# Performance work log

Hardware: AMD Instinct MI355X
Metric: run time of the kernel (lower is better)

## Reference

```python
import jax, jax.numpy as jnp
import numpy as np

C = 256
D = C // 4  # shared q/k projection dim = 64
EPS_BN = 1e-5


def _bn(x, g, b, m, v):
    # inference-style BatchNorm1d over channel dim of [B, C, N]
    inv = g / jnp.sqrt(v + EPS_BN)
    return x * inv[:, None] + (b - m * inv)[:, None]


def _sa_layer(x, xyz, qk_w, v_w, v_b, tr_w, tr_b, g, b, m, var):
    h = x + xyz                                             # [B,C,N]
    q = jnp.einsum('dc,bcn->bnd', qk_w, h)                  # [B,N,D]
    k = jnp.einsum('dc,bcn->bdn', qk_w, h)                  # [B,D,N] (shared weight)
    v = jnp.einsum('oc,bcn->bon', v_w, h) + v_b[:, None]    # [B,C,N]
    energy = jnp.einsum('bnd,bdm->bnm', q, k)               # [B,N,N]
    att = jax.nn.softmax(energy, axis=-1)
    # offset-attention L1 renorm over query dim (dim=1)
    att = att / (1e-9 + att.sum(axis=1, keepdims=True))
    x_r = jnp.einsum('bcn,bnm->bcm', v, att)                # [B,C,N]
    t = jnp.einsum('oc,bcn->bon', tr_w, x - x_r) + tr_b[:, None]
    return x + jax.nn.relu(_bn(t, g, b, m, var))


def setup_inputs() -> dict:
    key = jax.random.key(0)
    ks = jax.random.split(key, 20)
    B, N = 4, 4096
    inp = {
        'x': jax.random.normal(ks[0], (B, C, N), jnp.float32),
        'xyz': jax.random.normal(ks[1], (B, N, 3), jnp.float32),
        'pos_w': jax.random.normal(ks[2], (C, 3), jnp.float32) * 0.1,
        'pos_b': jax.random.normal(ks[3], (C,), jnp.float32) * 0.05,
        'conv1_w': jax.random.normal(ks[4], (C, C), jnp.float32) * (1.0 / np.sqrt(C)),
        'bn1_g': jax.random.uniform(ks[5], (C,), jnp.float32, 0.5, 1.5),
        'bn1_b': jax.random.normal(ks[6], (C,), jnp.float32) * 0.05,
        'bn1_m': jax.random.normal(ks[7], (C,), jnp.float32) * 0.05,
        'bn1_v': jax.random.uniform(ks[8], (C,), jnp.float32, 0.5, 1.5),
        # stacked params for 4 SA layers
        'qk_w': jax.random.normal(ks[9], (4, D, C), jnp.float32) * (1.0 / np.sqrt(C)),
        'v_w': jax.random.normal(ks[10], (4, C, C), jnp.float32) * (1.0 / np.sqrt(C)),
        'v_b': jax.random.normal(ks[11], (4, C), jnp.float32) * 0.05,
        'tr_w': jax.random.normal(ks[12], (4, C, C), jnp.float32) * (1.0 / np.sqrt(C)),
        'tr_b': jax.random.normal(ks[13], (4, C), jnp.float32) * 0.05,
        'bn_g': jax.random.uniform(ks[14], (4, C), jnp.float32, 0.5, 1.5),
        'bn_b': jax.random.normal(ks[15], (4, C), jnp.float32) * 0.05,
        'bn_m': jax.random.normal(ks[16], (4, C), jnp.float32) * 0.05,
        'bn_v': jax.random.uniform(ks[17], (4, C), jnp.float32, 0.5, 1.5),
    }
    return inp


def reference(x, xyz, pos_w, pos_b, conv1_w, bn1_g, bn1_b, bn1_m, bn1_v,
              qk_w, v_w, v_b, tr_w, tr_b, bn_g, bn_b, bn_m, bn_v):
    # xyz: [B,N,3] -> permute -> [B,3,N] -> pos conv -> [B,C,N]
    pos = jnp.einsum('oc,bnc->bon', pos_w, xyz) + pos_b[:, None]
    h = jnp.einsum('oc,bcn->bon', conv1_w, x)
    h = jax.nn.relu(_bn(h, bn1_g, bn1_b, bn1_m, bn1_v))
    outs = []
    for i in range(4):
        h = _sa_layer(h, pos, qk_w[i], v_w[i], v_b[i], tr_w[i], tr_b[i],
                      bn_g[i], bn_b[i], bn_m[i], bn_v[i])
        outs.append(h)
    return jnp.concatenate(outs, axis=1)  # [B, 4C, N]
```

## Files before the change

### kernel.cpp

```cpp
#include <hip/hip_runtime.h>

#define NB 4
#define NC 256
#define ND 64
#define NN 4096

typedef unsigned short us;
using short8v = __attribute__((ext_vector_type(8))) short;
using f32x4   = __attribute__((ext_vector_type(4))) float;

#define MFMA16 __builtin_amdgcn_mfma_f32_16x16x32_bf16

constexpr size_t SBCN = (size_t)NB * NC * NN;
constexpr size_t SBN  = (size_t)NB * NN;

__device__ inline us f2bf(float f) {
  unsigned u = __builtin_bit_cast(unsigned, f);
  u += 0x7fffu + ((u >> 16) & 1u);
  return (us)(u >> 16);
}
__device__ inline float bf2f(us s) {
  unsigned u = (unsigned)s << 16;
  return __builtin_bit_cast(float, u);
}
__device__ inline unsigned pack2(float a, float b) {
  return (unsigned)f2bf(a) | ((unsigned)f2bf(b) << 16);
}

__global__ __launch_bounds__(256) void pos_kernel(
    const float* __restrict__ xyz, const float* __restrict__ pw,
    const float* __restrict__ pb, float* __restrict__ pos)
{
  int idx = blockIdx.x * 256 + threadIdx.x;
  int n  = idx & (NN - 1);
  int tc = idx >> 12;
  int o  = tc & (NC - 1);
  int b  = tc >> 8;
  const float* xp = xyz + ((size_t)b * NN + n) * 3;
  pos[idx] = pb[o] + pw[o*3+0]*xp[0] + pw[o*3+1]*xp[1] + pw[o*3+2]*xp[2];
}

template<int O, bool ADD_P, bool HAS_BIAS, bool HAS_BN, bool RELU,
         bool HAS_RES, bool TRIPLE, bool VSPLIT, bool HAS_OUT2>
__global__ __launch_bounds__(256) void wgemm(
    const float* __restrict__ W, const float* __restrict__ H,
    const float* __restrict__ P, const float* __restrict__ bias,
    const float* __restrict__ bng, const float* __restrict__ bnb,
    const float* __restrict__ bnm, const float* __restrict__ bnv,
    const float* __restrict__ RES, float* __restrict__ OUT,
    float* __restrict__ OUT2, float* __restrict__ OUT3,
    float* __restrict__ OUT4)
{
  __shared__ float Wt[16][64];
  __shared__ float Ht[16][64];
  const int b  = blockIdx.z;
  const int o0 = blockIdx.y * 64;
  const int n0 = blockIdx.x * 64;
  const int t  = threadIdx.x;
  const int og = t >> 4, ng = t & 15;
  const int lo = t >> 2, lc4 = (t & 3) * 4;
  const int hc = t >> 4, hn4 = (t & 15) * 4;
  float acc[4][4] = {};
  for (int c0 = 0; c0 < NC; c0 += 16) {
    float4 w4 = *(const float4*)&W[(size_t)(o0 + lo) * NC + c0 + lc4];
    float4 h4 = *(const float4*)&H[((size_t)b * NC + c0 + hc) * NN + n0 + hn4];
    if (ADD_P) {
      float4 p4 = *(const float4*)&P[((size_t)b * NC + c0 + hc) * NN + n0 + hn4];
      h4.x += p4.x; h4.y += p4.y; h4.z += p4.z; h4.w += p4.w;
    }
    Wt[lc4+0][lo] = w4.x; Wt[lc4+1][lo] = w4.y;
    Wt[lc4+2][lo] = w4.z; Wt[lc4+3][lo] = w4.w;
    *(float4*)&Ht[hc][hn4] = h4;
    __syncthreads();
    #pragma unroll
    for (int cc = 0; cc < 16; ++cc) {
      float4 wv = *(const float4*)&Wt[cc][og*4];
      float4 hv = *(const float4*)&Ht[cc][ng*4];
      float wa[4] = {wv.x, wv.y, wv.z, wv.w};
      float ha[4] = {hv.x, hv.y, hv.z, hv.w};
      #pragma unroll
      for (int i = 0; i < 4; ++i)
        #pragma unroll
        for (int j = 0; j < 4; ++j)
          acc[i][j] += wa[i] * ha[j];
    }
    __syncthreads();
  }
  float vals[4][4];
  #pragma unroll
  for (int i = 0; i < 4; ++i) {
    const int o = o0 + og * 4 + i;
    float sc = 1.0f, sh = 0.0f;
    if (HAS_BIAS) sh = bias[o];
    if (HAS_BN) {
      float inv = bng[o] * rsqrtf(bnv[o] + 1e-5f);
      sh = sh * inv + (bnb[o] - bnm[o] * inv);
      sc = inv;
    }
    #pragma unroll
    for (int j = 0; j < 4; ++j) {
      float v = acc[i][j] * sc + sh;
      if (RELU) v = fmaxf(v, 0.0f);
      vals[i][j] = v;
    }
    if (HAS_RES) {
      float4 rv = *(const float4*)&RES[((size_t)b * NC + o) * NN + n0 + ng*4];
      vals[i][0] += rv.x; vals[i][1] += rv.y;
      vals[i][2] += rv.z; vals[i][3] += rv.w;
    }
  }
  if (TRIPLE) {
    us* o1 = (us*)OUT;  us* o2 = (us*)OUT2;  us* o3 = (us*)OUT3;
    #pragma unroll
    for (int j = 0; j < 4; ++j) {
      const int n = n0 + ng * 4 + j;
      us s1[4], s2[4], s3[4];
      #pragma unroll
      for (int i = 0; i < 4; ++i) {
        float v = vals[i][j];
        us h1 = f2bf(v); float r = v - bf2f(h1);
        us h2 = f2bf(r); r -= bf2f(h2);
        us h3 = f2bf(r);
        s1[i] = h1; s2[i] = h2; s3[i] = h3;
      }
      const size_t base = ((size_t)b * NN + n) * 64 + og * 4;
      uint2 u;
      u.x = (unsigned)s1[0] | ((unsigned)s1[1] << 16);
      u.y = (unsigned)s1[2] | ((unsigned)s1[3] << 16);
      *(uint2*)&o1[base] = u;
      u.x = (unsigned)s2[0] | ((unsigned)s2[1] << 16);
      u.y = (unsigned)s2[2] | ((unsigned)s2[3] << 16);
      *(uint2*)&o2[base] = u;
      u.x = (unsigned)s3[0] | ((unsigned)s3[1] << 16);
      u.y = (unsigned)s3[2] | ((unsigned)s3[3] << 16);
      *(uint2*)&o3[base] = u;
    }
  } else if (VSPLIT) {
    us* v1p = (us*)OUT; us* v2p = (us*)OUT2;
    #pragma unroll
    for (int i = 0; i < 4; ++i) {
      const int o = o0 + og * 4 + i;
      us s1[4], s2[4];
      #pragma unroll
      for (int j = 0; j < 4; ++j) {
        float v = vals[i][j];
        us h1 = f2bf(v);
        s1[j] = h1;
        s2[j] = f2bf(v - bf2f(h1));
      }
      const size_t base = ((size_t)b * NC + o) * NN + n0 + ng * 4;
      uint2 u;
      u.x = (unsigned)s1[0] | ((unsigned)s1[1] << 16);
      u.y = (unsigned)s1[2] | ((unsigned)s1[3] << 16);
      *(uint2*)&v1p[base] = u;
      u.x = (unsigned)s2[0] | ((unsigned)s2[1] << 16);
      u.y = (unsigned)s2[2] | ((unsigned)s2[3] << 16);
      *(uint2*)&v2p[base] = u;
    }
  } else {
    #pragma unroll
    for (int i = 0; i < 4; ++i) {
      const int o = o0 + og * 4 + i;
      float4 r = {vals[i][0], vals[i][1], vals[i][2], vals[i][3]};
      *(float4*)&OUT[((size_t)b * O + o) * NN + n0 + ng*4] = r;
      if (HAS_OUT2)
        *(float4*)&OUT2[((size_t)b * 4 * NC + o) * NN + n0 + ng*4] = r;
    }
  }
}

__global__ __launch_bounds__(128, 3) void rowstats_mfma(
    const us* __restrict__ q1, const us* __restrict__ q2,
    const us* __restrict__ q3,
    float* __restrict__ Mr, float* __restrict__ Lr)
{
  __shared__ us qs[3][32][72];
  const int b = blockIdx.y;
  const int n0 = blockIdx.x * 32;
  const int t = threadIdx.x;
  const int w = t >> 6, l = t & 63, lm = l & 15, g = l >> 4;
  const int nrow = n0 + w * 16;
  const us* qp[3] = {q1, q2, q3};
  short8v an[3][2];
  #pragma unroll
  for (int s = 0; s < 3; ++s) {
    const size_t ab = ((size_t)b * NN + nrow + lm) * ND + 8 * g;
    an[s][0] = *(const short8v*)(qp[s] + ab);
    an[s][1] = *(const short8v*)(qp[s] + ab + 32);
  }
  float mrun[4], lrun[4];
  #pragma unroll
  for (int r = 0; r < 4; ++r) { mrun[r] = -1e30f; lrun[r] = 0.f; }

  const int nloc0 = t >> 3, d8 = (t & 7) * 8;
  for (int m0 = 0; m0 < NN; m0 += 32) {
    __syncthreads();
    #pragma unroll
    for (int i = 0; i < 6; ++i) {
      const int s = i >> 1, n = (i & 1) * 16 + nloc0;
      *(short8v*)&qs[s][n][d8] =
          *(const short8v*)(qp[s] + ((size_t)b * NN + m0 + n) * ND + d8);
    }
    __syncthreads();
    float e[2][4];
    #pragma unroll
    for (int sub = 0; sub < 2; ++sub) {
      f32x4 eA = {0.f,0.f,0.f,0.f}, eB = {0.f,0.f,0.f,0.f};
      #pragma unroll
      for (int kh = 0; kh < 2; ++kh) {
        short8v b0 = *(const short8v*)&qs[0][sub*16+lm][kh*32+8*g];
        short8v b1 = *(const short8v*)&qs[1][sub*16+lm][kh*32+8*g];
        short8v b2 = *(const short8v*)&qs[2][sub*16+lm][kh*32+8*g];
        eA = MFMA16(an[0][kh], b0, eA, 0,0,0);
        eA = MFMA16(an[0][kh], b1, eA, 0,0,0);
        eA = MFMA16(an[0][kh], b2, eA, 0,0,0);
        eB = MFMA16(an[1][kh], b0, eB, 0,0,0);
        eB = MFMA16(an[2][kh], b0, eB, 0,0,0);
        eB = MFMA16(an[1][kh], b1, eB, 0,0,0);
      }
      f32x4 ee = eA + eB;
      #pragma unroll
      for (int r = 0; r < 4; ++r) e[sub][r] = ee[r];
    }
    #pragma unroll
    for (int r = 0; r < 4; ++r) {
      float mx = fmaxf(e[0][r], e[1][r]);
      float p = __expf(e[0][r] - mx) + __expf(e[1][r] - mx);
      float d = mx - mrun[r];
      if (d > 8.f) { lrun[r] = lrun[r] * __expf(-d) + p; mrun[r] = mx; }
      else          lrun[r] += p * __expf(d);
    }
  }
  #pragma unroll
  for (int r = 0; r < 4; ++r) {
    float m = mrun[r], s = lrun[r];
    #pragma unroll
    for (int off = 1; off < 16; off <<= 1) {
      float om = __shfl_xor(m, off);
      float os = __shfl_xor(s, off);
      float nm = fmaxf(m, om);
      s = s * __expf(m - nm) + os * __expf(om - nm);
      m = nm;
    }
    if (lm == 0) {
      Mr[(size_t)b * NN + nrow + 4 * g + r] = m;
      Lr[(size_t)b * NN + nrow + 4 * g + r] = 1.0f / s;
    }
  }
}

__global__ __launch_bounds__(256, 4) void fusedatt_mfma(
    const us* __restrict__ q1, const us* __restrict__ q2,
    const us* __restrict__ q3,
    const us* __restrict__ v1, const us* __restrict__ v2,
    const float* __restrict__ Mr, const float* __restrict__ Lr,
    float* __restrict__ xr, float* __restrict__ csb)
{
  __shared__ us qs[2][3][32][72];
  __shared__ us att1[64][40];
  __shared__ us att2[64][40];
  const int b  = blockIdx.y;
  const int m0 = blockIdx.x * 64;
  const int chalf = blockIdx.z & 1;
  const int nk    = blockIdx.z >> 1;
  const int c0 = chalf * 128;
  const int t  = threadIdx.x;
  const int w  = t >> 6, l = t & 63, lm = l & 15, g = l >> 4;
  const int mrow = w * 16 + lm;
  const int mg   = m0 + mrow;
  const us* qp[3] = {q1, q2, q3};

  short8v bm[3][2];
  #pragma unroll
  for (int s = 0; s < 3; ++s) {
    const size_t mb = ((size_t)b * NN + mg) * ND + 8 * g;
    bm[s][0] = *(const short8v*)(qp[s] + mb);
    bm[s][1] = *(const short8v*)(qp[s] + mb + 32);
  }
  const float* Mb = Mr + (size_t)b * NN;
  const float* Lb = Lr + (size_t)b * NN;
  const us* vb1 = v1 + ((size_t)b * NC + c0 + w * 32 + lm) * NN + 8 * g;
  const us* vb2 = v2 + ((size_t)b * NC + c0 + w * 32 + lm) * NN + 8 * g;

  f32x4 acc[2][4];
  const f32x4 fzero = {0.f,0.f,0.f,0.f};
  #pragma unroll
  for (int cs = 0; cs < 2; ++cs)
    #pragma unroll
    for (int mm = 0; mm < 4; ++mm) acc[cs][mm] = fzero;
  float csp = 0.f;

  const int nloc = t >> 3, d8 = (t & 7) * 8;
  const int nbeg = nk * (NN / 2), nend = nbeg + NN / 2;

  #pragma unroll
  for (int i = 0; i < 3; ++i)
    *(short8v*)&qs[0][i][nloc][d8] =
        *(const short8v*)(qp[i] + ((size_t)b * NN + nbeg + nloc) * ND + d8);
  __syncthreads();

  int cur = 0;
  for (int nt = nbeg; nt < nend; nt += 32) {
    short8v nx0, nx1, nx2;
    const bool has_next = (nt + 32) < nend;
    if (has_next) {
      const size_t nb = ((size_t)b * NN + nt + 32 + nloc) * ND + d8;
      nx0 = *(const short8v*)(qp[0] + nb);
      nx1 = *(const short8v*)(qp[1] + nb);
      nx2 = *(const short8v*)(qp[2] + nb);
    }
    #pragma unroll
    for (int sub = 0; sub < 2; ++sub) {
      f32x4 eA = fzero, eB = fzero;
      #pragma unroll
      for (int kh = 0; kh < 2; ++kh) {
        short8v a0 = *(const short8v*)&qs[cur][0][sub*16+lm][kh*32+8*g];
        short8v a1 = *(const short8v*)&qs[cur][1][sub*16+lm][kh*32+8*g];
        short8v a2 = *(const short8v*)&qs[cur][2][sub*16+lm][kh*32+8*g];
        eA = MFMA16(a0, bm[0][kh], eA, 0,0,0);
        eA = MFMA16(a0, bm[1][kh], eA, 0,0,0);
        eA = MFMA16(a0, bm[2][kh], eA, 0,0,0);
        eB = MFMA16(a1, bm[0][kh], eB, 0,0,0);
        eB = MFMA16(a2, bm[0][kh], eB, 0,0,0);
        eB = MFMA16(a1, bm[1][kh], eB, 0,0,0);
      }
      f32x4 ee = eA + eB;
      float m4[4], l4[4];
      *(float4*)m4 = *(const float4*)&Mb[nt + sub*16 + 4*g];
      *(float4*)l4 = *(const float4*)&Lb[nt + sub*16 + 4*g];
      us a1r[4], a2r[4];
      #pragma unroll
      for (int r = 0; r < 4; ++r) {
        float p = __expf(ee[r] - m4[r]) * l4[r];
        csp += p;
        us hi = f2bf(p);
        a1r[r] = hi;
        a2r[r] = f2bf(p - bf2f(hi));
      }
      uint2 u;
      u.x = (unsigned)a1r[0] | ((unsigned)a1r[1] << 16);
      u.y = (unsigned)a1r[2] | ((unsigned)a1r[3] << 16);
      *(uint2*)&att1[mrow][sub*16 + 4*g] = u;
      u.x = (unsigned)a2r[0] | ((unsigned)a2r[1] << 16);
      u.y = (unsigned)a2r[2] | ((unsigned)a2r[3] << 16);
      *(uint2*)&att2[mrow][sub*16 + 4*g] = u;
    }
    if (has_next) {
      *(short8v*)&qs[cur ^ 1][0][nloc][d8] = nx0;
      *(short8v*)&qs[cur ^ 1][1][nloc][d8] = nx1;
      *(short8v*)&qs[cur ^ 1][2][nloc][d8] = nx2;
    }
    __syncthreads();
    #pragma unroll
    for (int cs = 0; cs < 2; ++cs) {
      short8v av1 = *(const short8v*)(vb1 + (size_t)cs * 16 * NN + nt);
      short8v av2 = *(const short8v*)(vb2 + (size_t)cs * 16 * NN + nt);
      #pragma unroll
      for (int mm = 0; mm < 4; ++mm) {
        short8v batt1 = *(const short8v*)&att1[mm * 16 + lm][8 * g];
        short8v batt2 = *(const short8v*)&att2[mm * 16 + lm][8 * g];
        acc[cs][mm] = MFMA16(av1, batt1, acc[cs][mm], 0,0,0);
        acc[cs][mm] = MFMA16(av2, batt1, acc[cs][mm], 0,0,0);
        acc[cs][mm] = MFMA16(av1, batt2, acc[cs][mm], 0,0,0);
      }
    }
    __syncthreads();
    cur ^= 1;
  }

  csp += __shfl_xor(csp, 16);
  csp += __shfl_xor(csp, 32);
  if (chalf == 0 && l < 16)
    csb[(size_t)nk * SBN + (size_t)b * NN + m0 + w * 16 + l] = csp;

  float* xrp = xr + (size_t)nk * SBCN;
  #pragma unroll
  for (int cs = 0; cs < 2; ++cs) {
    #pragma unroll
    for (int mm = 0; mm < 4; ++mm) {
      #pragma unroll
      for (int r = 0; r < 4; ++r) {
        const int c = c0 + w * 32 + cs * 16 + 4 * g + r;
        const int m = m0 + mm * 16 + lm;
        xrp[((size_t)b * NC + c) * NN + m] = acc[cs][mm][r];
      }
    }
  }
}

__global__ __launch_bounds__(256) void xr_reduce(
    const float* __restrict__ xr, const float* __restrict__ csb,
    const float* __restrict__ h, float* __restrict__ dbuf)
{
  const int i4 = blockIdx.x * 256 + threadIdx.x;
  const int mq = i4 & (NN / 4 - 1);
  const int bc = i4 >> 10;
  const int b  = bc >> 8;
  const size_t off = (size_t)bc * NN + mq * 4;
  float4 a0 = *(const float4*)&xr[off];
  float4 a1 = *(const float4*)&xr[SBCN + off];
  float4 hv = *(const float4*)&h[off];
  const size_t co = (size_t)b * NN + mq * 4;
  float4 c0 = *(const float4*)&csb[co];
  float4 c1 = *(const float4*)&csb[SBN + co];
  float4 r;
  r.x = hv.x - (a0.x + a1.x) / (1e-9f + c0.x + c1.x);
  r.y = hv.y - (a0.y + a1.y) / (1e-9f + c0.y + c1.y);
  r.z = hv.z - (a0.z + a1.z) / (1e-9f + c0.z + c1.z);
  r.w = hv.w - (a0.w + a1.w) / (1e-9f + c0.w + c1.w);
  *(float4*)&dbuf[off] = r;
}

extern "C" void kernel_launch(void* const* d_in, const int* in_sizes, int n_in,
                              void* d_out, int out_size, void* d_ws, size_t ws_size,
                              hipStream_t stream) {
  const float* x      = (const float*)d_in[0];
  const float* xyz    = (const float*)d_in[1];
  const float* pos_w  = (const float*)d_in[2];
  const float* pos_b  = (const float*)d_in[3];
  const float* conv1w = (const float*)d_in[4];
  const float* bn1_g  = (const float*)d_in[5];
  const float* bn1_b  = (const float*)d_in[6];
  const float* bn1_m  = (const float*)d_in[7];
  const float* bn1_v  = (const float*)d_in[8];
  const float* qk_w   = (const float*)d_in[9];
  const float* v_w    = (const float*)d_in[10];
  const float* v_b    = (const float*)d_in[11];
  const float* tr_w   = (const float*)d_in[12];
  const float* tr_b   = (const float*)d_in[13];
  const float* bn_g   = (const float*)d_in[14];
  const float* bn_b   = (const float*)d_in[15];
  const float* bn_m   = (const float*)d_in[16];
  const float* bn_v   = (const float*)d_in[17];
  float* out = (float*)d_out;
  float* ws  = (float*)d_ws;

  const size_t BCN = SBCN;
  const size_t BDN = (size_t)NB * ND * NN;
  const size_t BN  = SBN;
  float* pos  = ws;
  float* h    = pos + BCN;
  float* xr   = h   + BCN;
  float* Mr   = xr  + 2 * BCN;
  float* Lr   = Mr  + BN;
  float* csb  = Lr  + BN;
  us* qA1 = (us*)(csb + 2 * BN);
  us* qA2 = qA1 + BDN;
  us* qA3 = qA2 + BDN;
  us* v1  = qA3 + BDN;
  us* v2  = v1  + BCN;

  pos_kernel<<<(NB * NC * NN) / 256, 256, 0, stream>>>(xyz, pos_w, pos_b, pos);

  wgemm<256, false, false, true, true, false, false, false, false>
      <<<dim3(NN/64, NC/64, NB), 256, 0, stream>>>(
          conv1w, x, nullptr, nullptr, bn1_g, bn1_b, bn1_m, bn1_v,
          nullptr, h, nullptr, nullptr, nullptr);

  for (int li = 0; li < 4; ++li) {
    const float* qw = qk_w + (size_t)li * ND * NC;
    const float* vw = v_w  + (size_t)li * NC * NC;
    const float* vb = v_b  + (size_t)li * NC;
    const float* tw = tr_w + (size_t)li * NC * NC;
    const float* tb = tr_b + (size_t)li * NC;

    wgemm<64, true, false, false, false, false, true, false, false>
        <<<dim3(NN/64, 1, NB), 256, 0, stream>>>(
            qw, h, pos, nullptr, nullptr, nullptr, nullptr, nullptr,
            nullptr, (float*)qA1, (float*)qA2, (float*)qA3, nullptr);

    wgemm<256, true, true, false, false, false, false, true, false>
        <<<dim3(NN/64, NC/64, NB), 256, 0, stream>>>(
            vw, h, pos, vb, nullptr, nullptr, nullptr, nullptr,
            nullptr, (float*)v1, (float*)v2, nullptr, nullptr);

    rowstats_mfma<<<dim3(NN/32, NB), 128, 0, stream>>>(qA1, qA2, qA3, Mr, Lr);

    fusedatt_mfma<<<dim3(NN/64, NB, 4), 256, 0, stream>>>(
        qA1, qA2, qA3, v1, v2, Mr, Lr, xr, csb);

    xr_reduce<<<(unsigned)(BCN / 1024), 256, 0, stream>>>(xr, csb, h, xr);

    wgemm<256, false, true, true, true, true, false, false, true>
        <<<dim3(NN/64, NC/64, NB), 256, 0, stream>>>(
            tw, xr, nullptr, tb, bn_g + li*NC, bn_b + li*NC,
            bn_m + li*NC, bn_v + li*NC,
            h, h, out + (size_t)li * NC * NN, nullptr, nullptr);
  }
}
```

Baseline: 1.850 ms.

## Move q/v/trans projections to bf16x3 split MFMA GEMMs with fused splits

Replaces the fp32 SIMT tiled GEMMs for the q, v and trans projections with an MFMA kernel. It uses three-way bf16 splits of both weights and activations, with six cross-product MFMAs per tile to keep near-fp32 accuracy. Weights are split once up front. Activations are transposed and split into n-major bf16 buffers by a new tsplit kernel, and that kernel absorbs the old xr_reduce normalization. The trans GEMM epilogue writes h and the output slice, and also emits the split (h+pos) operand for the next layer, aliasing the xr workspace. The cost is extra split-buffer memory traffic and a few extra launches, in exchange for running the projection math on matrix cores instead of vector FMAs.

```diff
diff --git a/kernel.cpp b/kernel.cpp
--- a/kernel.cpp
+++ b/kernel.cpp
@@ -22,9 +22,6 @@
 __device__ inline float bf2f(us s) {
   unsigned u = (unsigned)s << 16;
   return __builtin_bit_cast(float, u);
-}
-__device__ inline unsigned pack2(float a, float b) {
-  return (unsigned)f2bf(a) | ((unsigned)f2bf(b) << 16);
 }
 
 __global__ __launch_bounds__(256) void pos_kernel(
@@ -40,16 +37,11 @@
   pos[idx] = pb[o] + pw[o*3+0]*xp[0] + pw[o*3+1]*xp[1] + pw[o*3+2]*xp[2];
 }
 
-template<int O, bool ADD_P, bool HAS_BIAS, bool HAS_BN, bool RELU,
-         bool HAS_RES, bool TRIPLE, bool VSPLIT, bool HAS_OUT2>
-__global__ __launch_bounds__(256) void wgemm(
+__global__ __launch_bounds__(256) void wgemm_conv1(
     const float* __restrict__ W, const float* __restrict__ H,
-    const float* __restrict__ P, const float* __restrict__ bias,
     const float* __restrict__ bng, const float* __restrict__ bnb,
     const float* __restrict__ bnm, const float* __restrict__ bnv,
-    const float* __restrict__ RES, float* __restrict__ OUT,
-    float* __restrict__ OUT2, float* __restrict__ OUT3,
-    float* __restrict__ OUT4)
+    float* __restrict__ OUT)
 {
   __shared__ float Wt[16][64];
   __shared__ float Ht[16][64];
@@ -64,10 +56,6 @@
   for (int c0 = 0; c0 < NC; c0 += 16) {
     float4 w4 = *(const float4*)&W[(size_t)(o0 + lo) * NC + c0 + lc4];
     float4 h4 = *(const float4*)&H[((size_t)b * NC + c0 + hc) * NN + n0 + hn4];
-    if (ADD_P) {
-      float4 p4 = *(const float4*)&P[((size_t)b * NC + c0 + hc) * NN + n0 + hn4];
-      h4.x += p4.x; h4.y += p4.y; h4.z += p4.z; h4.w += p4.w;
-    }
     Wt[lc4+0][lo] = w4.x; Wt[lc4+1][lo] = w4.y;
     Wt[lc4+2][lo] = w4.z; Wt[lc4+3][lo] = w4.w;
     *(float4*)&Ht[hc][hn4] = h4;
@@ -86,44 +74,158 @@
     }
     __syncthreads();
   }
-  float vals[4][4];
   #pragma unroll
   for (int i = 0; i < 4; ++i) {
     const int o = o0 + og * 4 + i;
-    float sc = 1.0f, sh = 0.0f;
-    if (HAS_BIAS) sh = bias[o];
-    if (HAS_BN) {
-      float inv = bng[o] * rsqrtf(bnv[o] + 1e-5f);
-      sh = sh * inv + (bnb[o] - bnm[o] * inv);
-      sc = inv;
-    }
-    #pragma unroll
-    for (int j = 0; j < 4; ++j) {
-      float v = acc[i][j] * sc + sh;
-      if (RELU) v = fmaxf(v, 0.0f);
-      vals[i][j] = v;
-    }
-    if (HAS_RES) {
-      float4 rv = *(const float4*)&RES[((size_t)b * NC + o) * NN + n0 + ng*4];
-      vals[i][0] += rv.x; vals[i][1] += rv.y;
-      vals[i][2] += rv.z; vals[i][3] += rv.w;
-    }
-  }
-  if (TRIPLE) {
-    us* o1 = (us*)OUT;  us* o2 = (us*)OUT2;  us* o3 = (us*)OUT3;
-    #pragma unroll
-    for (int j = 0; j < 4; ++j) {
-      const int n = n0 + ng * 4 + j;
+    float inv = bng[o] * rsqrtf(bnv[o] + 1e-5f);
+    float sh = bnb[o] - bnm[o] * inv;
+    float4 r;
+    r.x = fmaxf(acc[i][0]*inv + sh, 0.f);
+    r.y = fmaxf(acc[i][1]*inv + sh, 0.f);
+    r.z = fmaxf(acc[i][2]*inv + sh, 0.f);
+    r.w = fmaxf(acc[i][3]*inv + sh, 0.f);
+    *(float4*)&OUT[((size_t)b * NC + o) * NN + n0 + ng*4] = r;
+  }
+}
+
+__global__ __launch_bounds__(256) void wsplit(
+    const float* __restrict__ src, us* __restrict__ d1,
+    us* __restrict__ d2, us* __restrict__ d3, int ntot)
+{
+  int i = blockIdx.x * 256 + threadIdx.x;
+  if (i >= ntot) return;
+  float v = src[i];
+  us h1 = f2bf(v); float r = v - bf2f(h1);
+  us h2 = f2bf(r); r -= bf2f(h2);
+  us h3 = f2bf(r);
+  d1[i] = h1; d2[i] = h2; d3[i] = h3;
+}
+
+template<bool FROM_XR>
+__global__ __launch_bounds__(256) void tsplit(
+    const float* __restrict__ h, const float* __restrict__ pos,
+    const float* __restrict__ xr, const float* __restrict__ csb,
+    us* __restrict__ o1, us* __restrict__ o2, us* __restrict__ o3)
+{
+  __shared__ float tile[64][69];
+  __shared__ float cf[64];
+  const int b = blockIdx.z, c0 = blockIdx.y * 64, n0 = blockIdx.x * 64;
+  const int t = threadIdx.x;
+  if (FROM_XR) {
+    if (t < 64) {
+      const size_t co = (size_t)b * NN + n0 + t;
+      cf[t] = 1.0f / (1e-9f + csb[co] + csb[SBN + co]);
+    }
+    __syncthreads();
+  }
+  #pragma unroll
+  for (int p = 0; p < 4; ++p) {
+    const int c = p * 16 + (t >> 4), n4 = (t & 15) * 4;
+    const size_t off = ((size_t)b * NC + c0 + c) * NN + n0 + n4;
+    float4 hv = *(const float4*)&h[off];
+    float v0, v1, v2, v3;
+    if (FROM_XR) {
+      float4 a0 = *(const float4*)&xr[off];
+      float4 a1 = *(const float4*)&xr[SBCN + off];
+      v0 = hv.x - (a0.x + a1.x) * cf[n4+0];
+      v1 = hv.y - (a0.y + a1.y) * cf[n4+1];
+      v2 = hv.z - (a0.z + a1.z) * cf[n4+2];
+      v3 = hv.w - (a0.w + a1.w) * cf[n4+3];
+    } else {
+      float4 pv = *(const float4*)&pos[off];
+      v0 = hv.x + pv.x; v1 = hv.y + pv.y;
+      v2 = hv.z + pv.z; v3 = hv.w + pv.w;
+    }
+    tile[c][n4+0] = v0; tile[c][n4+1] = v1;
+    tile[c][n4+2] = v2; tile[c][n4+3] = v3;
+  }
+  __syncthreads();
+  const int w = t >> 6, l = t & 63;
+  const int n = w * 16 + (l >> 2), cq = (l & 3) * 16;
+  #pragma unroll
+  for (int j = 0; j < 4; ++j) {
+    const int c4 = cq + j * 4;
+    us s1[4], s2[4], s3[4];
+    #pragma unroll
+    for (int i = 0; i < 4; ++i) {
+      float v = tile[c4 + i][n];
+      us h1 = f2bf(v); float r = v - bf2f(h1);
+      us h2 = f2bf(r); r -= bf2f(h2);
+      s1[i] = h1; s2[i] = h2; s3[i] = f2bf(r);
+    }
+    const size_t base = ((size_t)b * NN + n0 + n) * NC + c0 + c4;
+    uint2 u;
+    u.x = (unsigned)s1[0] | ((unsigned)s1[1] << 16);
+    u.y = (unsigned)s1[2] | ((unsigned)s1[3] << 16);
+    *(uint2*)&o1[base] = u;
+    u.x = (unsigned)s2[0] | ((unsigned)s2[1] << 16);
+    u.y = (unsigned)s2[2] | ((unsigned)s2[3] << 16);
+    *(uint2*)&o2[base] = u;
+    u.x = (unsigned)s3[0] | ((unsigned)s3[1] << 16);
+    u.y = (unsigned)s3[2] | ((unsigned)s3[3] << 16);
+    *(uint2*)&o3[base] = u;
+  }
+}
+
+template<bool QOUT, bool VOUT, bool TROUT>
+__global__ __launch_bounds__(256, 4) void mgemm(
+    const us* __restrict__ w1, const us* __restrict__ w2,
+    const us* __restrict__ w3,
+    const us* __restrict__ i1, const us* __restrict__ i2,
+    const us* __restrict__ i3,
+    const float* __restrict__ bias,
+    const float* __restrict__ bng, const float* __restrict__ bnb,
+    const float* __restrict__ bnm, const float* __restrict__ bnv,
+    const float* __restrict__ RES, const float* __restrict__ pos,
+    float* __restrict__ hout, float* __restrict__ outsl,
+    us* __restrict__ o1, us* __restrict__ o2, us* __restrict__ o3)
+{
+  const int b  = blockIdx.z;
+  const int o0 = blockIdx.y * 64;
+  const int n0 = blockIdx.x * 64;
+  const int t  = threadIdx.x;
+  const int w  = t >> 6, l = t & 63, lm = l & 15, g = l >> 4;
+  const int n  = n0 + w * 16 + lm;
+  const size_t ibase = ((size_t)b * NN + n) * 256 + 8 * g;
+
+  f32x4 acc[4];
+  const f32x4 fzero = {0.f,0.f,0.f,0.f};
+  #pragma unroll
+  for (int osub = 0; osub < 4; ++osub) acc[osub] = fzero;
+
+  #pragma unroll
+  for (int kh = 0; kh < 8; ++kh) {
+    const int ko = kh * 32;
+    short8v bh1 = *(const short8v*)(i1 + ibase + ko);
+    short8v bh2 = *(const short8v*)(i2 + ibase + ko);
+    short8v bh3 = *(const short8v*)(i3 + ibase + ko);
+    #pragma unroll
+    for (int osub = 0; osub < 4; ++osub) {
+      const size_t wb = (size_t)(o0 + osub * 16 + lm) * 256 + ko + 8 * g;
+      short8v aw1 = *(const short8v*)(w1 + wb);
+      short8v aw2 = *(const short8v*)(w2 + wb);
+      short8v aw3 = *(const short8v*)(w3 + wb);
+      acc[osub] = MFMA16(aw1, bh1, acc[osub], 0,0,0);
+      acc[osub] = MFMA16(aw1, bh2, acc[osub], 0,0,0);
+      acc[osub] = MFMA16(aw2, bh1, acc[osub], 0,0,0);
+      acc[osub] = MFMA16(aw1, bh3, acc[osub], 0,0,0);
+      acc[osub] = MFMA16(aw2, bh2, acc[osub], 0,0,0);
+      acc[osub] = MFMA16(aw3, bh1, acc[osub], 0,0,0);
+    }
+  }
+
+  #pragma unroll
+  for (int osub = 0; osub < 4; ++osub) {
+    if (QOUT) {
       us s1[4], s2[4], s3[4];
       #pragma unroll
-      for (int i = 0; i < 4; ++i) {
-        float v = vals[i][j];
-        us h1 = f2bf(v); float r = v - bf2f(h1);
-        us h2 = f2bf(r); r -= bf2f(h2);
-        us h3 = f2bf(r);
-        s1[i] = h1; s2[i] = h2; s3[i] = h3;
-      }
-      const size_t base = ((size_t)b * NN + n) * 64 + og * 4;
+      for (int r = 0; r < 4; ++r) {
+        float v = acc[osub][r];
+        us h1 = f2bf(v); float rr = v - bf2f(h1);
+        us h2 = f2bf(rr); rr -= bf2f(h2);
+        s1[r] = h1; s2[r] = h2; s3[r] = f2bf(rr);
+      }
+      const size_t base = ((size_t)b * NN + n) * 64 + osub * 16 + 4 * g;
       uint2 u;
       u.x = (unsigned)s1[0] | ((unsigned)s1[1] << 16);
       u.y = (unsigned)s1[2] | ((unsigned)s1[3] << 16);
@@ -134,37 +236,43 @@
       u.x = (unsigned)s3[0] | ((unsigned)s3[1] << 16);
       u.y = (unsigned)s3[2] | ((unsigned)s3[3] << 16);
       *(uint2*)&o3[base] = u;
-    }
-  } else if (VSPLIT) {
-    us* v1p = (us*)OUT; us* v2p = (us*)OUT2;
-    #pragma unroll
-    for (int i = 0; i < 4; ++i) {
-      const int o = o0 + og * 4 + i;
-      us s1[4], s2[4];
-      #pragma unroll
-      for (int j = 0; j < 4; ++j) {
-        float v = vals[i][j];
+    } else if (VOUT) {
+      #pragma unroll
+      for (int r = 0; r < 4; ++r) {
+        const int c = o0 + osub * 16 + 4 * g + r;
+        float v = acc[osub][r] + bias[c];
         us h1 = f2bf(v);
-        s1[j] = h1;
-        s2[j] = f2bf(v - bf2f(h1));
-      }
-      const size_t base = ((size_t)b * NC + o) * NN + n0 + ng * 4;
+        const size_t off = ((size_t)b * NC + c) * NN + n;
+        o1[off] = h1;
+        o2[off] = f2bf(v - bf2f(h1));
+      }
+    } else {
+      us s1[4], s2[4], s3[4];
+      #pragma unroll
+      for (int r = 0; r < 4; ++r) {
+        const int c = o0 + osub * 16 + 4 * g + r;
+        const size_t off = ((size_t)b * NC + c) * NN + n;
+        float inv = bng[c] * rsqrtf(bnv[c] + 1e-5f);
+        float sh = bias[c] * inv + (bnb[c] - bnm[c] * inv);
+        float val = fmaxf(acc[osub][r] * inv + sh, 0.f) + RES[off];
+        hout[off] = val;
+        outsl[((size_t)b * 4 * NC + c) * NN + n] = val;
+        float hpv = val + pos[off];
+        us h1 = f2bf(hpv); float rr = hpv - bf2f(h1);
+        us h2 = f2bf(rr); rr -= bf2f(h2);
+        s1[r] = h1; s2[r] = h2; s3[r] = f2bf(rr);
+      }
+      const size_t base = ((size_t)b * NN + n) * NC + o0 + osub * 16 + 4 * g;
       uint2 u;
       u.x = (unsigned)s1[0] | ((unsigned)s1[1] << 16);
       u.y = (unsigned)s1[2] | ((unsigned)s1[3] << 16);
-      *(uint2*)&v1p[base] = u;
+      *(uint2*)&o1[base] = u;
       u.x = (unsigned)s2[0] | ((unsigned)s2[1] << 16);
       u.y = (unsigned)s2[2] | ((unsigned)s2[3] << 16);
-      *(uint2*)&v2p[base] = u;
-    }
-  } else {
-    #pragma unroll
-    for (int i = 0; i < 4; ++i) {
-      const int o = o0 + og * 4 + i;
-      float4 r = {vals[i][0], vals[i][1], vals[i][2], vals[i][3]};
-      *(float4*)&OUT[((size_t)b * O + o) * NN + n0 + ng*4] = r;
-      if (HAS_OUT2)
-        *(float4*)&OUT2[((size_t)b * 4 * NC + o) * NN + n0 + ng*4] = r;
+      *(uint2*)&o2[base] = u;
+      u.x = (unsigned)s3[0] | ((unsigned)s3[1] << 16);
+      u.y = (unsigned)s3[2] | ((unsigned)s3[3] << 16);
+      *(uint2*)&o3[base] = u;
     }
   }
 }
@@ -386,29 +494,6 @@
       }
     }
   }
-}
-
-__global__ __launch_bounds__(256) void xr_reduce(
-    const float* __restrict__ xr, const float* __restrict__ csb,
-    const float* __restrict__ h, float* __restrict__ dbuf)
-{
-  const int i4 = blockIdx.x * 256 + threadIdx.x;
-  const int mq = i4 & (NN / 4 - 1);
-  const int bc = i4 >> 10;
-  const int b  = bc >> 8;
-  const size_t off = (size_t)bc * NN + mq * 4;
-  float4 a0 = *(const float4*)&xr[off];
-  float4 a1 = *(const float4*)&xr[SBCN + off];
-  float4 hv = *(const float4*)&h[off];
-  const size_t co = (size_t)b * NN + mq * 4;
-  float4 c0 = *(const float4*)&csb[co];
-  float4 c1 = *(const float4*)&csb[SBN + co];
-  float4 r;
-  r.x = hv.x - (a0.x + a1.x) / (1e-9f + c0.x + c1.x);
-  r.y = hv.y - (a0.y + a1.y) / (1e-9f + c0.y + c1.y);
-  r.z = hv.z - (a0.z + a1.z) / (1e-9f + c0.z + c1.z);
-  r.w = hv.w - (a0.w + a1.w) / (1e-9f + c0.w + c1.w);
-  *(float4*)&dbuf[off] = r;
 }
 
 extern "C" void kernel_launch(void* const* d_in, const int* in_sizes, int n_in,
@@ -438,6 +523,9 @@
   const size_t BCN = SBCN;
   const size_t BDN = (size_t)NB * ND * NN;
   const size_t BN  = SBN;
+  const int WQ = 4 * 64 * 256;
+  const int WV = 4 * 256 * 256;
+
   float* pos  = ws;
   float* h    = pos + BCN;
   float* xr   = h   + BCN;
@@ -449,42 +537,51 @@
   us* qA3 = qA2 + BDN;
   us* v1  = qA3 + BDN;
   us* v2  = v1  + BCN;
+  us* db1 = v2  + BCN;
+  us* db2 = db1 + BCN;
+  us* db3 = db2 + BCN;
+  us* wq1 = db3 + BCN;  us* wq2 = wq1 + WQ;  us* wq3 = wq2 + WQ;
+  us* wv1 = wq3 + WQ;   us* wv2 = wv1 + WV;  us* wv3 = wv2 + WV;
+  us* wt1 = wv3 + WV;   us* wt2 = wt1 + WV;  us* wt3 = wt2 + WV;
+  us* hp1 = (us*)xr;
+  us* hp2 = hp1 + BCN;
+  us* hp3 = hp2 + BCN;
 
   pos_kernel<<<(NB * NC * NN) / 256, 256, 0, stream>>>(xyz, pos_w, pos_b, pos);
 
-  wgemm<256, false, false, true, true, false, false, false, false>
-      <<<dim3(NN/64, NC/64, NB), 256, 0, stream>>>(
-          conv1w, x, nullptr, nullptr, bn1_g, bn1_b, bn1_m, bn1_v,
-          nullptr, h, nullptr, nullptr, nullptr);
+  wgemm_conv1<<<dim3(NN/64, NC/64, NB), 256, 0, stream>>>(
+      conv1w, x, bn1_g, bn1_b, bn1_m, bn1_v, h);
+
+  wsplit<<<WQ/256, 256, 0, stream>>>(qk_w, wq1, wq2, wq3, WQ);
+  wsplit<<<WV/256, 256, 0, stream>>>(v_w,  wv1, wv2, wv3, WV);
+  wsplit<<<WV/256, 256, 0, stream>>>(tr_w, wt1, wt2, wt3, WV);
+
+  tsplit<false><<<dim3(NN/64, NC/64, NB), 256, 0, stream>>>(
+      h, pos, nullptr, nullptr, hp1, hp2, hp3);
 
   for (int li = 0; li < 4; ++li) {
-    const float* qw = qk_w + (size_t)li * ND * NC;
-    const float* vw = v_w  + (size_t)li * NC * NC;
-    const float* vb = v_b  + (size_t)li * NC;
-    const float* tw = tr_w + (size_t)li * NC * NC;
-    const float* tb = tr_b + (size_t)li * NC;
-
-    wgemm<64, true, false, false, false, false, true, false, false>
-        <<<dim3(NN/64, 1, NB), 256, 0, stream>>>(
-            qw, h, pos, nullptr, nullptr, nullptr, nullptr, nullptr,
-            nullptr, (float*)qA1, (float*)qA2, (float*)qA3, nullptr);
-
-    wgemm<256, true, true, false, false, false, false, true, false>
-        <<<dim3(NN/64, NC/64, NB), 256, 0, stream>>>(
-            vw, h, pos, vb, nullptr, nullptr, nullptr, nullptr,
-            nullptr, (float*)v1, (float*)v2, nullptr, nullptr);
+    mgemm<true, false, false><<<dim3(NN/64, 1, NB), 256, 0, stream>>>(
+        wq1 + li*64*256, wq2 + li*64*256, wq3 + li*64*256,
+        hp1, hp2, hp3, nullptr, nullptr, nullptr, nullptr, nullptr,
+        nullptr, nullptr, nullptr, nullptr, qA1, qA2, qA3);
+
+    mgemm<false, true, false><<<dim3(NN/64, NC/64, NB), 256, 0, stream>>>(
+        wv1 + li*256*256, wv2 + li*256*256, wv3 + li*256*256,
+        hp1, hp2, hp3, v_b + li*NC, nullptr, nullptr, nullptr, nullptr,
+        nullptr, nullptr, nullptr, nullptr, v1, v2, nullptr);
 
     rowstats_mfma<<<dim3(NN/32, NB), 128, 0, stream>>>(qA1, qA2, qA3, Mr, Lr);
 
     fusedatt_mfma<<<dim3(NN/64, NB, 4), 256, 0, stream>>>(
         qA1, qA2, qA3, v1, v2, Mr, Lr, xr, csb);
 
-    xr_reduce<<<(unsigned)(BCN / 1024), 256, 0, stream>>>(xr, csb, h, xr);
-
-    wgemm<256, false, true, true, true, true, false, false, true>
-        <<<dim3(NN/64, NC/64, NB), 256, 0, stream>>>(
-            tw, xr, nullptr, tb, bn_g + li*NC, bn_b + li*NC,
-            bn_m + li*NC, bn_v + li*NC,
-            h, h, out + (size_t)li * NC * NN, nullptr, nullptr);
-  }
-}
+    tsplit<true><<<dim3(NN/64, NC/64, NB), 256, 0, stream>>>(
+        h, nullptr, xr, csb, db1, db2, db3);
+
+    mgemm<false, false, true><<<dim3(NN/64, NC/64, NB), 256, 0, stream>>>(
+        wt1 + li*256*256, wt2 + li*256*256, wt3 + li*256*256,
+        db1, db2, db3, tr_b + li*NC,
+        bn_g + li*NC, bn_b + li*NC, bn_m + li*NC, bn_v + li*NC,
+        h, pos, h, out + (size_t)li * NC * NN, hp1, hp2, hp3);
+  }
+}
```

Result: slower. 2.138 ms (+15.5%).
